# Kernel optimization log

Measured on AMD Instinct MI355X. Metric: run time of the kernel, lower is better.

The kernel has to match this reference:

```python
import jax, jax.numpy as jnp
import numpy as np

CENTER_LR = 0.5  # default center_lr in _compute_centroids_mb


def setup_inputs() -> dict:
    key = jax.random.key(0)
    k1, k2, k3 = jax.random.split(key, 3)
    N, D, K = 16384, 1024, 1024
    embedded = jax.random.normal(k1, (N, D), dtype=jnp.float32)
    centers = jax.random.normal(k2, (K, D), dtype=jnp.float32)
    count = jax.random.randint(k3, (K,), 0, 10000, dtype=jnp.int32)
    return {"embedded": embedded, "centers": centers, "count": count}


def _sq_euclidean(x, c):
    # ||x - c||^2 via expansion; avoids materializing [N, K, D]
    x2 = jnp.sum(x * x, axis=1, keepdims=True)        # [N, 1]
    c2 = jnp.sum(c * c, axis=1)[None, :]              # [1, K]
    d = x2 + c2 - 2.0 * (x @ c.T)                     # [N, K]
    return jnp.maximum(d, 0.0)


def reference(embedded, centers, count):
    N, D = embedded.shape
    K = centers.shape[0]
    # predict_hard: argmin of squared euclidean distance
    dist = _sq_euclidean(embedded, centers)           # [N, K]
    labels = jnp.argmin(dist, axis=1)                 # [N]
    # _int_to_one_hot assignment matrix
    A = jax.nn.one_hot(labels, K, dtype=embedded.dtype)  # [N, K]
    # segmented reduction: batch_cluster_sums[k] = sum_{i: label_i=k} embedded[i]
    # (embedded is detached in the original -> stop_gradient)
    batch_cluster_sums = jnp.einsum('nk,nd->kd', A, jax.lax.stop_gradient(embedded))  # [K, D]
    mask_sum = jnp.sum(A, axis=0)                     # [K]
    nonzero = mask_sum != 0                           # [K]
    # count EMA (only for clusters present in the batch)
    cc = count.astype(jnp.float32)
    cc_new = jnp.where(nonzero, (1.0 - CENTER_LR) * cc + CENTER_LR * mask_sum, cc)
    per_center_lr = 1.0 / (cc_new + 1.0)              # [K]
    batch_centers = batch_cluster_sums / jnp.where(nonzero, mask_sum, 1.0)[:, None]
    new_centers = jnp.where(
        nonzero[:, None],
        (1.0 - per_center_lr)[:, None] * centers + per_center_lr[:, None] * batch_centers,
        centers,
    )
    return new_centers
```

## Files before the change

### kernel.cpp

```cpp
#include <hip/hip_runtime.h>

typedef __attribute__((ext_vector_type(8))) short bf16x8;
typedef __attribute__((ext_vector_type(4))) float f32x4;

__device__ __forceinline__ unsigned short f2bf(float f) {
    unsigned u = __float_as_uint(f);
    unsigned r = (u + 0x7FFFu + ((u >> 16) & 1u)) >> 16;
    return (unsigned short)r;
}

__device__ __forceinline__ void gload16(const unsigned short* g, unsigned short* l) {
    __builtin_amdgcn_global_load_lds((const __attribute__((address_space(1))) void*)g,
                                     (__attribute__((address_space(3))) void*)l, 16, 0, 0);
}

#define BARRIER() do { asm volatile("" ::: "memory"); __builtin_amdgcn_s_barrier(); asm volatile("" ::: "memory"); } while (0)


__global__ void conv_x_kernel(const float* __restrict__ x, unsigned short* __restrict__ xb, int total8) {
    int i = blockIdx.x * blockDim.x + threadIdx.x;
    if (i >= total8) return;
    const float4* xv = (const float4*)x;
    float4 a = xv[(size_t)i * 2];
    float4 b = xv[(size_t)i * 2 + 1];
    uint4 o;
    o.x = (unsigned)f2bf(a.x) | ((unsigned)f2bf(a.y) << 16);
    o.y = (unsigned)f2bf(a.z) | ((unsigned)f2bf(a.w) << 16);
    o.z = (unsigned)f2bf(b.x) | ((unsigned)f2bf(b.y) << 16);
    o.w = (unsigned)f2bf(b.z) | ((unsigned)f2bf(b.w) << 16);
    ((uint4*)xb)[i] = o;
}

__global__ void conv_c_kernel(const float* __restrict__ c, unsigned short* __restrict__ cb,
                              float* __restrict__ c2, unsigned long long* __restrict__ packed,
                              int N, int D) {
    int k = blockIdx.x;
    int tid = threadIdx.x;
    const float4 v = ((const float4*)(c + (long)k * D))[tid];
    uint2 o;
    o.x = (unsigned)f2bf(v.x) | ((unsigned)f2bf(v.y) << 16);
    o.y = (unsigned)f2bf(v.z) | ((unsigned)f2bf(v.w) << 16);
    ((uint2*)(cb + (long)k * D))[tid] = o;
    float s = v.x * v.x + v.y * v.y + v.z * v.z + v.w * v.w;
    #pragma unroll
    for (int d = 1; d < 64; d <<= 1) s += __shfl_xor(s, d, 64);
    __shared__ float wsum[4];
    int lane = tid & 63, w = tid >> 6;
    if (lane == 0) wsum[w] = s;
    __syncthreads();
    if (tid == 0) c2[k] = wsum[0] + wsum[1] + wsum[2] + wsum[3];
    int gid = k * 256 + tid;
    if (gid < N) packed[gid] = ~0ull;
}

__global__ void __launch_bounds__(512, 2)
gemm_argmin_kernel(const unsigned short* __restrict__ Xb,
                   const unsigned short* __restrict__ Cb,
                   const float* __restrict__ c2,
                   unsigned long long* __restrict__ packed,
                   int D, int nt) {
    __shared__ unsigned short sh[65536];
    const int tid  = threadIdx.x;
    const int lane = tid & 63;
    const int w    = tid >> 6;
    const int wr   = w >> 2;
    const int wc   = w & 3;
    const long rowbase = (long)blockIdx.x * 256;
    const int  colbase = blockIdx.y * 256;
    const int fr = lane & 15;
    const int g  = lane >> 4;

    const int c0 = tid, c1 = 512 + tid;
    const unsigned short* gA0 = Xb + (rowbase + (c0 >> 2)) * D + (c0 & 3) * 8;
    const unsigned short* gA1 = Xb + (rowbase + (c1 >> 2)) * D + (c1 & 3) * 8;
    const unsigned short* gB0 = Cb + ((long)colbase + (c0 >> 2)) * D + (c0 & 3) * 8;
    const unsigned short* gB1 = Cb + ((long)colbase + (c1 >> 2)) * D + (c1 & 3) * 8;

    f32x4 acc[8][4] = {};
    bf16x8 a[8], b[4];

    auto stage = [&](int kt) {
        const int s = (kt & 3) * 8192;
        const long ko = (long)kt * 32;
        gload16(gA0 + ko, sh + s + c0 * 8);
        gload16(gA1 + ko, sh + s + c1 * 8);
        gload16(gB0 + ko, sh + 32768 + s + c0 * 8);
        gload16(gB1 + ko, sh + 32768 + s + c1 * 8);
    };

    stage(0); stage(1); stage(2);
    asm volatile("s_waitcnt vmcnt(8)" ::: "memory");
    BARRIER();

    for (int t = 0; t < nt; ++t) {
        const int sb = (t & 3) * 8192;
        if (t + 3 < nt) stage(t + 3);
        const int ar = sb + (wr * 128 + fr) * 32 + g * 8;
        #pragma unroll
        for (int m = 0; m < 8; ++m) a[m] = *(const bf16x8*)&sh[ar + m * 512];
        const int br = 32768 + sb + (wc * 64 + fr) * 32 + g * 8;
        #pragma unroll
        for (int n = 0; n < 4; ++n) b[n] = *(const bf16x8*)&sh[br + n * 512];
        asm volatile("s_waitcnt vmcnt(8) lgkmcnt(0)" ::: "memory");
        BARRIER();
        __builtin_amdgcn_s_setprio(1);
        #pragma unroll
        for (int m = 0; m < 8; ++m)
            #pragma unroll
            for (int n = 0; n < 4; ++n)
                acc[m][n] = __builtin_amdgcn_mfma_f32_16x16x32_bf16(a[m], b[n], acc[m][n], 0, 0, 0);
        __builtin_amdgcn_s_setprio(0);
    }

    float c2v[4];
    int   kcol[4];
    #pragma unroll
    for (int n = 0; n < 4; ++n) {
        kcol[n] = colbase + wc * 64 + n * 16 + fr;
        c2v[n]  = c2[kcol[n]];
    }
    #pragma unroll
    for (int m = 0; m < 8; ++m) {
        #pragma unroll
        for (int reg = 0; reg < 4; ++reg) {
            unsigned long long best = ~0ull;
            #pragma unroll
            for (int n = 0; n < 4; ++n) {
                float score = c2v[n] - 2.0f * acc[m][n][reg];
                unsigned u = __float_as_uint(score);
                u ^= (u >> 31) ? 0xFFFFFFFFu : 0x80000000u;
                unsigned long long cand = ((unsigned long long)u << 32) | (unsigned)kcol[n];
                best = cand < best ? cand : best;
            }
            #pragma unroll
            for (int s = 1; s < 16; s <<= 1) {
                unsigned long long other = __shfl_xor(best, s, 64);
                best = other < best ? other : best;
            }
            if (fr == 0) {
                long row = rowbase + wr * 128 + m * 16 + g * 4 + reg;
                atomicMin(&packed[row], best);
            }
        }
    }
}

__global__ void extract16_kernel(const unsigned long long* __restrict__ p,
                                 unsigned short* __restrict__ lab, int n) {
    int i = blockIdx.x * blockDim.x + threadIdx.x;
    if (i < n) lab[i] = (unsigned short)(p[i] & 0xFFFFull);
}

__global__ void segsum_partial_kernel(const unsigned short* __restrict__ lab,
                                      const float* __restrict__ emb,
                                      float* __restrict__ partial,
                                      int* __restrict__ pcount,
                                      int N, int D) {
    const int k   = blockIdx.x;
    const int s   = blockIdx.y;
    const int tid = threadIdx.x;
    const int grp = tid >> 8;
    const int ct  = tid & 255;
    const int lane = tid & 63, w = tid >> 6;

    __shared__ int idxbuf[4096];
    __shared__ int cnts[16];
    __shared__ float4 red[4][256];

    const int slice = N >> 2;
    const int base0 = s * slice;
    int total = 0;
    for (int base = base0; base < base0 + slice; base += 1024) {
        const int n = base + tid;
        const bool m = (lab[n] == (unsigned short)k);
        const unsigned long long bal = __ballot(m);
        if (lane == 0) cnts[w] = (int)__popcll(bal);
        __syncthreads();
        int myoff = total, run = total;
        #pragma unroll
        for (int w2 = 0; w2 < 16; ++w2) {
            if (w2 == w) myoff = run;
            run += cnts[w2];
        }
        if (m) idxbuf[myoff + (int)__popcll(bal & ((1ull << lane) - 1ull))] = n;
        total = run;
        __syncthreads();
    }

    float4 acc = {0.f, 0.f, 0.f, 0.f};
    for (int j = grp; j < total; j += 4) {
        const int row = idxbuf[j];
        const float4 v = *(const float4*)(emb + (long)row * D + ct * 4);
        acc.x += v.x; acc.y += v.y; acc.z += v.z; acc.w += v.w;
    }
    red[grp][ct] = acc;
    __syncthreads();
    if (grp == 0) {
        float4 r = red[0][ct];
        #pragma unroll
        for (int q = 1; q < 4; ++q) {
            const float4 v = red[q][ct];
            r.x += v.x; r.y += v.y; r.z += v.z; r.w += v.w;
        }
        *(float4*)(partial + ((long)(k * 4 + s)) * D + ct * 4) = r;
    }
    if (tid == 0) pcount[k * 4 + s] = total;
}

__global__ void finalize_kernel(const float* __restrict__ partial,
                                const int* __restrict__ pcount,
                                const float* __restrict__ centers,
                                const int* __restrict__ cnt,
                                float* __restrict__ out, int D) {
    const int k = blockIdx.x;
    const int ct = threadIdx.x;
    float4 acc = {0.f, 0.f, 0.f, 0.f};
    int mtot = 0;
    #pragma unroll
    for (int s = 0; s < 4; ++s) {
        const float4 p = *(const float4*)(partial + ((long)(k * 4 + s)) * D + ct * 4);
        acc.x += p.x; acc.y += p.y; acc.z += p.z; acc.w += p.w;
        mtot += pcount[k * 4 + s];
    }
    const float4 cv = *(const float4*)(centers + (long)k * D + ct * 4);
    float4 o;
    if (mtot > 0) {
        float ccn = 0.5f * (float)cnt[k] + 0.5f * (float)mtot;
        float lr  = 1.0f / (ccn + 1.0f);
        float im  = 1.0f / (float)mtot;
        float om  = 1.0f - lr;
        o.x = om * cv.x + lr * (acc.x * im);
        o.y = om * cv.y + lr * (acc.y * im);
        o.z = om * cv.z + lr * (acc.z * im);
        o.w = om * cv.w + lr * (acc.w * im);
    } else {
        o = cv;
    }
    *(float4*)(out + (long)k * D + ct * 4) = o;
}


extern "C" void kernel_launch(void* const* d_in, const int* in_sizes, int n_in,
                              void* d_out, int out_size, void* d_ws, size_t ws_size,
                              hipStream_t stream) {
    const float* emb = (const float*)d_in[0];
    const float* cen = (const float*)d_in[1];
    const int*   cnt = (const int*)d_in[2];
    float* out = (float*)d_out;
    const int K = in_sizes[2];
    const int D = in_sizes[1] / K;
    const int N = in_sizes[0] / D;

    char* ws = (char*)d_ws;
    size_t xb_bytes = (size_t)N * D * 2;
    size_t cb_bytes = (size_t)K * D * 2;
    unsigned short* Xb = (unsigned short*)ws;
    unsigned short* Cb = (unsigned short*)(ws + xb_bytes);
    float* c2 = (float*)(ws + xb_bytes + cb_bytes);
    unsigned long long* packed = (unsigned long long*)(ws + xb_bytes + cb_bytes + (size_t)K * 4);
    unsigned short* lab16 = (unsigned short*)(ws + xb_bytes + cb_bytes + (size_t)K * 4 + (size_t)N * 8);
    int* pcount = (int*)(ws + xb_bytes + cb_bytes + (size_t)K * 4 + (size_t)N * 8 + (size_t)N * 2);
    float* partial = (float*)ws;

    int total8 = N * D / 8;
    conv_x_kernel<<<dim3((total8 + 255) / 256), dim3(256), 0, stream>>>(emb, Xb, total8);
    conv_c_kernel<<<dim3(K), dim3(256), 0, stream>>>(cen, Cb, c2, packed, N, D);
    gemm_argmin_kernel<<<dim3(N / 256, K / 256), dim3(512), 0, stream>>>(Xb, Cb, c2, packed, D, D / 32);
    extract16_kernel<<<dim3((N + 255) / 256), dim3(256), 0, stream>>>(packed, lab16, N);
    segsum_partial_kernel<<<dim3(K, 4), dim3(1024), 0, stream>>>(lab16, emb, partial, pcount, N, D);
    finalize_kernel<<<dim3(K), dim3(256), 0, stream>>>(partial, pcount, cen, cnt, out, D);
}
```

Measured before the change: 101.3 us.

## Restructure GEMM-argmin pipeline with swizzled LDS, register-staged A and triple buffering

The GEMM main loop is rewritten so A tiles are loaded through registers and stored to LDS with an XOR swizzle. B tiles keep direct global-to-LDS loads but use a swizzled layout, and the ring drops from four to three stages, cutting LDS from 128KB to 96KB. Half of the A fragments for the next tile are prefetched from LDS during the current tile's MFMAs, and the loop count becomes a template constant so it can be fully unrolled with a peeled epilogue. The aim is to remove LDS bank conflicts and overlap LDS reads with MFMA work. The cost is higher register pressure and more complex hand-tuned synchronization.

```diff
diff --git a/kernel.cpp b/kernel.cpp
--- a/kernel.cpp
+++ b/kernel.cpp
@@ -53,13 +53,14 @@
     if (gid < N) packed[gid] = ~0ull;
 }
 
+template<int NT>
 __global__ void __launch_bounds__(512, 2)
 gemm_argmin_kernel(const unsigned short* __restrict__ Xb,
                    const unsigned short* __restrict__ Cb,
                    const float* __restrict__ c2,
                    unsigned long long* __restrict__ packed,
-                   int D, int nt) {
-    __shared__ unsigned short sh[65536];
+                   int D) {
+    __shared__ unsigned short sh[49152];
     const int tid  = threadIdx.x;
     const int lane = tid & 63;
     const int w    = tid >> 6;
@@ -67,50 +68,101 @@
     const int wc   = w & 3;
     const long rowbase = (long)blockIdx.x * 256;
     const int  colbase = blockIdx.y * 256;
-    const int fr = lane & 15;
-    const int g  = lane >> 4;
-
-    const int c0 = tid, c1 = 512 + tid;
-    const unsigned short* gA0 = Xb + (rowbase + (c0 >> 2)) * D + (c0 & 3) * 8;
-    const unsigned short* gA1 = Xb + (rowbase + (c1 >> 2)) * D + (c1 & 3) * 8;
-    const unsigned short* gB0 = Cb + ((long)colbase + (c0 >> 2)) * D + (c0 & 3) * 8;
-    const unsigned short* gB1 = Cb + ((long)colbase + (c1 >> 2)) * D + (c1 & 3) * 8;
+    const int fr = lane & 15, g = lane >> 4;
+
+    const int sphys = ((fr & 1) * 4 + g) ^ (fr >> 1);
+    const int abase = wr * 4096 + (fr >> 1) * 64 + sphys * 8;
+    const int bbase = 24576 + wc * 2048 + (fr >> 1) * 64 + sphys * 8;
+
+    const int ac0 = 2 * tid, ac1 = 2 * tid + 1;
+    const int arow0 = ac0 >> 2, aq0 = ac0 & 3;
+    const int arow1 = ac1 >> 2, aq1 = ac1 & 3;
+    const unsigned short* gA0 = Xb + (rowbase + arow0) * D + aq0 * 8;
+    const unsigned short* gA1 = Xb + (rowbase + arow1) * D + aq1 * 8;
+    const int awr0 = (arow0 >> 1) * 64 + ((((arow0 & 1) * 4 + aq0) ^ ((arow0 >> 1) & 7)) * 8);
+    const int awr1 = (arow1 >> 1) * 64 + ((((arow1 & 1) * 4 + aq1) ^ ((arow1 >> 1) & 7)) * 8);
+
+    const int p0 = w * 128 + lane, p1 = w * 128 + 64 + lane;
+    const int l0 = p0 >> 3, sl0 = (p0 & 7) ^ (l0 & 7);
+    const int l1 = p1 >> 3, sl1 = (p1 & 7) ^ (l1 & 7);
+    const unsigned short* gB0 = Cb + ((long)colbase + l0 * 2 + (sl0 >> 2)) * D + (sl0 & 3) * 8;
+    const unsigned short* gB1 = Cb + ((long)colbase + l1 * 2 + (sl1 >> 2)) * D + (sl1 & 3) * 8;
 
     f32x4 acc[8][4] = {};
-    bf16x8 a[8], b[4];
-
-    auto stage = [&](int kt) {
-        const int s = (kt & 3) * 8192;
-        const long ko = (long)kt * 32;
-        gload16(gA0 + ko, sh + s + c0 * 8);
-        gload16(gA1 + ko, sh + s + c1 * 8);
-        gload16(gB0 + ko, sh + 32768 + s + c0 * 8);
-        gload16(gB1 + ko, sh + 32768 + s + c1 * 8);
+    bf16x8 a03A[4], a03B[4], a47[4], b[4];
+    uint4 aregA[2], aregB[2];
+
+    auto loadA = [&](int kt, uint4 (&r)[2]) {
+        r[0] = *(const uint4*)(gA0 + (long)kt * 32);
+        r[1] = *(const uint4*)(gA1 + (long)kt * 32);
     };
-
-    stage(0); stage(1); stage(2);
-    asm volatile("s_waitcnt vmcnt(8)" ::: "memory");
+    auto writeA = [&](int kt, uint4 (&r)[2]) {
+        const int s = (kt % 3) * 8192;
+        *(uint4*)&sh[s + awr0] = r[0];
+        *(uint4*)&sh[s + awr1] = r[1];
+    };
+    auto gloadB = [&](int kt) {
+        const int s = 24576 + (kt % 3) * 8192;
+        gload16(gB0 + (long)kt * 32, sh + s + (w * 128) * 8);
+        gload16(gB1 + (long)kt * 32, sh + s + (w * 128 + 64) * 8);
+    };
+
+    loadA(0, aregA);
+    gloadB(0);
+    loadA(1, aregB);
+    gloadB(1);
+    writeA(0, aregA);
+    loadA(2, aregA);
+    writeA(1, aregB);
+    asm volatile("s_waitcnt lgkmcnt(0)" ::: "memory");
     BARRIER();
-
-    for (int t = 0; t < nt; ++t) {
-        const int sb = (t & 3) * 8192;
-        if (t + 3 < nt) stage(t + 3);
-        const int ar = sb + (wr * 128 + fr) * 32 + g * 8;
-        #pragma unroll
-        for (int m = 0; m < 8; ++m) a[m] = *(const bf16x8*)&sh[ar + m * 512];
-        const int br = 32768 + sb + (wc * 64 + fr) * 32 + g * 8;
-        #pragma unroll
-        for (int n = 0; n < 4; ++n) b[n] = *(const bf16x8*)&sh[br + n * 512];
-        asm volatile("s_waitcnt vmcnt(8) lgkmcnt(0)" ::: "memory");
-        BARRIER();
+    #pragma unroll
+    for (int m = 0; m < 4; ++m) a03A[m] = *(const bf16x8*)&sh[abase + m * 512];
+
+    auto tile = [&](int t, bf16x8 (&acur)[4], bf16x8 (&anxt)[4],
+                    uint4 (&wreg)[2], uint4 (&lreg)[2],
+                    bool doB, bool doA, bool doW, bool doAhead, bool vm0, bool doBar) {
+        const int sb = (t % 3) * 8192;
+        if (doB) gloadB(t + 2);
+        if (doA) loadA(t + 3, lreg);
+        #pragma unroll
+        for (int n = 0; n < 4; ++n) b[n] = *(const bf16x8*)&sh[bbase + sb + n * 512];
+        #pragma unroll
+        for (int m = 0; m < 4; ++m) a47[m] = *(const bf16x8*)&sh[abase + sb + (m + 4) * 512];
+        if (doAhead) {
+            const int sn = ((t + 1) % 3) * 8192;
+            #pragma unroll
+            for (int m = 0; m < 4; ++m) anxt[m] = *(const bf16x8*)&sh[abase + sn + m * 512];
+        }
         __builtin_amdgcn_s_setprio(1);
         #pragma unroll
-        for (int m = 0; m < 8; ++m)
+        for (int m = 0; m < 4; ++m)
             #pragma unroll
             for (int n = 0; n < 4; ++n)
-                acc[m][n] = __builtin_amdgcn_mfma_f32_16x16x32_bf16(a[m], b[n], acc[m][n], 0, 0, 0);
+                acc[m][n] = __builtin_amdgcn_mfma_f32_16x16x32_bf16(acur[m], b[n], acc[m][n], 0, 0, 0);
+        #pragma unroll
+        for (int m = 0; m < 4; ++m)
+            #pragma unroll
+            for (int n = 0; n < 4; ++n)
+                acc[m + 4][n] = __builtin_amdgcn_mfma_f32_16x16x32_bf16(a47[m], b[n], acc[m + 4][n], 0, 0, 0);
         __builtin_amdgcn_s_setprio(0);
-    }
+        if (doW) writeA(t + 2, wreg);
+        if (vm0) asm volatile("s_waitcnt vmcnt(0)" ::: "memory");
+        if (doBar) {
+            asm volatile("s_waitcnt lgkmcnt(0)" ::: "memory");
+            BARRIER();
+        }
+    };
+
+    for (int tp = 0; tp < (NT - 4) / 2; ++tp) {
+        const int t = tp * 2;
+        tile(t,     a03A, a03B, aregA, aregB, true, true, true, true, false, true);
+        tile(t + 1, a03B, a03A, aregB, aregA, true, true, true, true, false, true);
+    }
+    tile(NT - 4, a03A, a03B, aregA, aregB, true,  true,  true,  true,  false, true);
+    tile(NT - 3, a03B, a03A, aregB, aregA, true,  false, true,  true,  false, true);
+    tile(NT - 2, a03A, a03B, aregA, aregB, false, false, false, true,  true,  true);
+    tile(NT - 1, a03B, a03A, aregB, aregA, false, false, false, false, false, false);
 
     float c2v[4];
     int   kcol[4];
@@ -265,7 +317,7 @@
     int total8 = N * D / 8;
     conv_x_kernel<<<dim3((total8 + 255) / 256), dim3(256), 0, stream>>>(emb, Xb, total8);
     conv_c_kernel<<<dim3(K), dim3(256), 0, stream>>>(cen, Cb, c2, packed, N, D);
-    gemm_argmin_kernel<<<dim3(N / 256, K / 256), dim3(512), 0, stream>>>(Xb, Cb, c2, packed, D, D / 32);
+    gemm_argmin_kernel<32><<<dim3(N / 256, K / 256), dim3(512), 0, stream>>>(Xb, Cb, c2, packed, D);
     extract16_kernel<<<dim3((N + 255) / 256), dim3(256), 0, stream>>>(packed, lab16, N);
     segsum_partial_kernel<<<dim3(K, 4), dim3(1024), 0, stream>>>(lab16, emb, partial, pcount, N, D);
     finalize_kernel<<<dim3(K), dim3(256), 0, stream>>>(partial, pcount, cen, cnt, out, D);
```

Measured after the change: 118.2 us. +16.7%, slower.
